# Kernel optimization log

Measured on AMD Instinct MI355X. Metric: run time of the kernel, lower is better.

The kernel has to match this reference:

```python
import jax, jax.numpy as jnp
import numpy as np

D_MODEL, D_K, D_FF, N = 1024, 128, 4096, 8192

def _linear_params(key, fan_in, fan_out):
    # mimic torch nn.Linear default init (uniform +/- 1/sqrt(fan_in))
    k1, k2 = jax.random.split(key)
    bound = 1.0 / np.sqrt(fan_in)
    W = jax.random.uniform(k1, (fan_out, fan_in), jnp.float32, -bound, bound)
    b = jax.random.uniform(k2, (fan_out,), jnp.float32, -bound, bound)
    return W, b

def setup_inputs() -> dict:
    key = jax.random.key(0)
    ks = jax.random.split(key, 7)
    x = jax.random.normal(ks[0], (N, D_MODEL), jnp.float32)
    Wq, bq = _linear_params(ks[1], D_MODEL, D_K)
    Wk, bk = _linear_params(ks[2], D_MODEL, D_K)
    Wv, bv = _linear_params(ks[3], D_MODEL, D_K)
    Wp, bp = _linear_params(ks[4], D_K, D_MODEL)
    W1, b1 = _linear_params(ks[5], D_MODEL, D_FF)
    W2, b2 = _linear_params(ks[6], D_FF, D_MODEL)
    return {"x": x, "Wq": Wq, "bq": bq, "Wk": Wk, "bk": bk, "Wv": Wv, "bv": bv,
            "Wp": Wp, "bp": bp, "W1": W1, "b1": b1, "W2": W2, "b2": b2}

def reference(x, Wq, bq, Wk, bk, Wv, bv, Wp, bp, W1, b1, W2, b2):
    # projections (torch Linear: x @ W.T + b)
    Q = x @ Wq.T + bq            # [n, d_k]
    K = x @ Wk.T + bk            # [n, d_k]
    V = x @ Wv.T + bv            # [n, d_k]
    # linear attention, original evaluation order: (Q @ K^T) @ V
    attn = Q @ K.T               # [n, n]
    context = attn @ V           # [n, d_k]
    out = context @ Wp.T + bp    # [n, d_model]
    x = x + out                  # residual 1
    h = jax.nn.relu(x @ W1.T + b1)  # [n, d_ff]
    return x + (h @ W2.T + b2)   # residual 2
```

## Files before the change

### kernel.cpp

```cpp
#include <hip/hip_runtime.h>


#define MROWS 8192
#define DMODEL 1024
#define DK 128
#define DFF 4096

typedef __attribute__((ext_vector_type(8))) __bf16 bf16x8;
typedef __attribute__((ext_vector_type(4))) float f32x4;

#define BAR()     __builtin_amdgcn_s_barrier()
#define WAITV(n)  asm volatile("s_waitcnt vmcnt(" #n ")" ::: "memory")
#define LGKMC(n)  asm volatile("s_waitcnt lgkmcnt(" #n ")" ::: "memory")
#define SCHED0()  __builtin_amdgcn_sched_barrier(0)
#define GLOAD(src, dst) __builtin_amdgcn_global_load_lds( \
    (const __attribute__((address_space(1))) void*)(src), \
    (__attribute__((address_space(3))) void*)(dst), 16, 0, 0)

#define LDSO(p) ((unsigned)(unsigned long long) \
    (__attribute__((address_space(3))) const char*)(const char*)(p))

__device__ __forceinline__ bf16x8 ldsr(unsigned off) {
    bf16x8 r;
    asm volatile("ds_read_b128 %0, %1" : "=v"(r) : "v"(off));
    return r;
}

__global__ __launch_bounds__(256) void cast_f32_bf16(
    const float* __restrict__ src, __bf16* __restrict__ dst, int n8)
{
    for (int i = blockIdx.x * blockDim.x + threadIdx.x; i < n8;
         i += gridDim.x * blockDim.x) {
        const float4 a = reinterpret_cast<const float4*>(src)[2 * i];
        const float4 b = reinterpret_cast<const float4*>(src)[2 * i + 1];
        bf16x8 o;
        o[0] = (__bf16)a.x; o[1] = (__bf16)a.y; o[2] = (__bf16)a.z; o[3] = (__bf16)a.w;
        o[4] = (__bf16)b.x; o[5] = (__bf16)b.y; o[6] = (__bf16)b.z; o[7] = (__bf16)b.w;
        reinterpret_cast<bf16x8*>(dst)[i] = o;
    }
}

__device__ __forceinline__ void cast_one(const float* s, __bf16* d, int i) {
    const float4 a = reinterpret_cast<const float4*>(s)[2 * i];
    const float4 b = reinterpret_cast<const float4*>(s)[2 * i + 1];
    bf16x8 o;
    o[0] = (__bf16)a.x; o[1] = (__bf16)a.y; o[2] = (__bf16)a.z; o[3] = (__bf16)a.w;
    o[4] = (__bf16)b.x; o[5] = (__bf16)b.y; o[6] = (__bf16)b.z; o[7] = (__bf16)b.w;
    reinterpret_cast<bf16x8*>(d)[i] = o;
}

__global__ __launch_bounds__(256) void cast6(
    const float* __restrict__ s0, __bf16* __restrict__ d0,
    const float* __restrict__ s1, __bf16* __restrict__ d1,
    const float* __restrict__ s2, __bf16* __restrict__ d2,
    const float* __restrict__ s3, __bf16* __restrict__ d3,
    const float* __restrict__ s4, __bf16* __restrict__ d4,
    const float* __restrict__ s5, __bf16* __restrict__ d5)
{
    const int b = blockIdx.x, t = threadIdx.x;
    if      (b <  64)  cast_one(s0, d0, b * 256 + t);
    else if (b < 128)  cast_one(s1, d1, (b - 64) * 256 + t);
    else if (b < 192)  cast_one(s2, d2, (b - 128) * 256 + t);
    else if (b < 256)  cast_one(s3, d3, (b - 192) * 256 + t);
    else if (b < 2304) cast_one(s4, d4, (b - 256) * 256 + t);
    else               cast_one(s5, d5, (b - 2304) * 256 + t);
}

__global__ void pack_bias3(const float* __restrict__ a, const float* __restrict__ b,
                           const float* __restrict__ c, float* __restrict__ o)
{
    const int t = threadIdx.x;
    o[t] = a[t]; o[128 + t] = b[t]; o[256 + t] = c[t];
}

__global__ __launch_bounds__(256) void ffn2_reduce(
    float* __restrict__ y, const __bf16* __restrict__ P0,
    const __bf16* __restrict__ P1, const float* __restrict__ b2, int n8)
{
    for (int i = blockIdx.x * blockDim.x + threadIdx.x; i < n8;
         i += gridDim.x * blockDim.x) {
        const int col0 = (i << 3) & (DMODEL - 1);
        const float4 ba = *reinterpret_cast<const float4*>(&b2[col0]);
        const float4 bb = *reinterpret_cast<const float4*>(&b2[col0 + 4]);
        float4 o0 = reinterpret_cast<const float4*>(y)[2 * i];
        float4 o1 = reinterpret_cast<const float4*>(y)[2 * i + 1];
        const bf16x8 p0 = reinterpret_cast<const bf16x8*>(P0)[i];
        const bf16x8 p1 = reinterpret_cast<const bf16x8*>(P1)[i];
        o0.x += (float)p0[0] + (float)p1[0] + ba.x;
        o0.y += (float)p0[1] + (float)p1[1] + ba.y;
        o0.z += (float)p0[2] + (float)p1[2] + ba.z;
        o0.w += (float)p0[3] + (float)p1[3] + ba.w;
        o1.x += (float)p0[4] + (float)p1[4] + bb.x;
        o1.y += (float)p0[5] + (float)p1[5] + bb.y;
        o1.z += (float)p0[6] + (float)p1[6] + bb.z;
        o1.w += (float)p0[7] + (float)p1[7] + bb.w;
        reinterpret_cast<float4*>(y)[2 * i]     = o0;
        reinterpret_cast<float4*>(y)[2 * i + 1] = o1;
    }
}

template<bool RELU, bool RESID, bool BIAS, bool OUTBF, bool DUAL>
__global__ __launch_bounds__(256) void gemm128(
    const __bf16* __restrict__ A, int lda,
    const __bf16* __restrict__ W,
    const float* __restrict__ bias,
    const float* __restrict__ resid,
    void* __restrict__ Cout, __bf16* __restrict__ Cbf, int ldc, int K)
{
    constexpr int BK = 32;
    __shared__ __bf16 As[128 * BK];
    __shared__ __bf16 Bs[128 * BK];

    const int tid  = threadIdx.x;
    const int lane = tid & 63;
    const int w    = tid >> 6;
    const int wm   = w >> 1;
    const int wn   = w & 1;
    const int fr   = lane & 15;
    const int fq   = lane >> 4;

    const long row0 = (long)blockIdx.y * 128;
    const long col0 = (long)blockIdx.x * 128;

    const int sr = (w << 4) + (lane >> 2);
    const int sc = (lane & 3) << 3;

    const __bf16* gA0 = A + (row0 + sr) * (long)lda + sc;
    const __bf16* gA1 = A + (row0 + 64 + sr) * (long)lda + sc;
    const __bf16* gW0 = W + (col0 + sr) * (long)K + sc;
    const __bf16* gW1 = W + (col0 + 64 + sr) * (long)K + sc;

    __bf16* lA0 = &As[(w << 4) * BK];
    __bf16* lA1 = &As[((w << 4) + 64) * BK];
    __bf16* lB0 = &Bs[(w << 4) * BK];
    __bf16* lB1 = &Bs[((w << 4) + 64) * BK];

    f32x4 acc[4][4] = {};

    for (int k0 = 0; k0 < K; k0 += BK) {
        GLOAD(gA0 + k0, lA0);
        GLOAD(gA1 + k0, lA1);
        GLOAD(gW0 + k0, lB0);
        GLOAD(gW1 + k0, lB1);
        __syncthreads();

        bf16x8 af[4], bfr[4];
        #pragma unroll
        for (int m = 0; m < 4; m++)
            af[m] = *reinterpret_cast<const bf16x8*>(
                &As[(wm * 64 + m * 16 + fr) * BK + fq * 8]);
        #pragma unroll
        for (int n = 0; n < 4; n++)
            bfr[n] = *reinterpret_cast<const bf16x8*>(
                &Bs[(wn * 64 + n * 16 + fr) * BK + fq * 8]);

        #pragma unroll
        for (int m = 0; m < 4; m++)
            #pragma unroll
            for (int n = 0; n < 4; n++)
                acc[m][n] = __builtin_amdgcn_mfma_f32_16x16x32_bf16(
                    af[m], bfr[n], acc[m][n], 0, 0, 0);
        __syncthreads();
    }

    float bc[4];
    #pragma unroll
    for (int n = 0; n < 4; n++)
        bc[n] = BIAS ? bias[col0 + wn * 64 + n * 16 + fr] : 0.0f;
    #pragma unroll
    for (int m = 0; m < 4; m++) {
        #pragma unroll
        for (int j = 0; j < 4; j++) {
            const long r = row0 + wm * 64 + m * 16 + fq * 4 + j;
            #pragma unroll
            for (int n = 0; n < 4; n++) {
                const long c = col0 + wn * 64 + n * 16 + fr;
                float v = acc[m][n][j] + bc[n];
                if constexpr (RESID) v += resid[r * ldc + c];
                if constexpr (RELU)  v = fmaxf(v, 0.0f);
                if constexpr (OUTBF) ((__bf16*)Cout)[r * ldc + c] = (__bf16)v;
                else                 ((float*)Cout)[r * ldc + c] = v;
                if constexpr (DUAL)  Cbf[r * ldc + c] = (__bf16)v;
            }
        }
    }
}

#define RD_B()                                             \
    _Pragma("unroll")                                      \
    for (int n = 0; n < 4; n++) {                          \
        bb[n][0] = ldsr(pB + rb0 + n * 2048);              \
        bb[n][1] = ldsr(pB + rb1 + n * 2048);              \
    }
#define RD_A(m0_, cnt_)                                    \
    _Pragma("unroll")                                      \
    for (int m = m0_; m < m0_ + cnt_; m++) {               \
        a[m][0] = ldsr(pA + rb0 + m * 2048);               \
        a[m][1] = ldsr(pA + rb1 + m * 2048);               \
    }
#define MFMA2(m0_)                                                            \
    _Pragma("unroll")                                                         \
    for (int m = m0_; m < m0_ + 2; m++)                                       \
        _Pragma("unroll")                                                     \
        for (int n = 0; n < 4; n++) {                                         \
            acc[m][n] = __builtin_amdgcn_mfma_f32_16x16x32_bf16(              \
                a[m][0], bb[n][0], acc[m][n], 0, 0, 0);                       \
            acc[m][n] = __builtin_amdgcn_mfma_f32_16x16x32_bf16(              \
                a[m][1], bb[n][1], acc[m][n], 0, 0, 0);                       \
        }

template<bool RELU, bool BIAS>
__global__ __launch_bounds__(256, 2) void gemm256x128(
    const __bf16* __restrict__ A, int lda,
    const __bf16* __restrict__ W, int ldw,
    const float* __restrict__ bias,
    __bf16* __restrict__ Cout, long sstride, int ldc,
    int klen, int nb, int nbx)
{
    __shared__ char lds[49152];

    const int bid = blockIdx.x;
    const int sid = bid / nb;
    const int ib  = bid % nb;
    const int chunk = nb >> 3;
    const int swz   = (ib & 7) * chunk + (ib >> 3);
    const int bx    = swz % nbx;
    const int by    = swz / nbx;

    const long row0 = (long)by * 256;
    const long col0 = (long)bx * 128;

    const __bf16* Ash = A + (long)sid * klen;
    const __bf16* Wsh = W + (long)sid * klen;

    const int tid  = threadIdx.x;
    const int lane = tid & 63;
    const int w    = tid >> 6;
    const int wm   = w >> 1;
    const int wn   = w & 1;
    const int fr   = lane & 15;
    const int fq   = lane >> 4;

    const int scole = ((lane & 7) ^ (lane >> 3)) << 3;
    const __bf16* gA = Ash + (row0 + w * 8 + (lane >> 3)) * (long)lda + scole;
    const __bf16* gB = Wsh + (col0 + w * 8 + (lane >> 3)) * (long)ldw + scole;

    char* ldsc = &lds[0];
    const unsigned lbase = LDSO(ldsc);
    const int nt = klen >> 6;

    auto stage = [&](int t) {
        const __bf16* ap = gA + (long)t * 64;
        const __bf16* bp = gB + (long)t * 64;
        #pragma unroll
        for (int r = 0; r < 8; r++)
            GLOAD(ap + (long)(32 * r) * lda, ldsc + r * 4096 + (w << 10));
        #pragma unroll
        for (int r = 0; r < 4; r++)
            GLOAD(bp + (long)(32 * r) * ldw, ldsc + 32768 + r * 4096 + (w << 10));
    };

    const unsigned rb0 = fr * 128 + ((fq * 16) ^ ((fr & 7) << 4));
    const unsigned rb1 = fr * 128 + ((64 + fq * 16) ^ ((fr & 7) << 4));
    const unsigned pA = lbase + (wm << 14);
    const unsigned pB = lbase + 32768 + (wn << 13);

    f32x4 acc[8][4] = {};
    bf16x8 a[8][2], bb[4][2];

    for (int t = 0; t < nt; ++t) {
        stage(t);
        WAITV(0);
        BAR();

        RD_B();
        RD_A(0, 8);

        LGKMC(12); SCHED0();
        __builtin_amdgcn_s_setprio(1); MFMA2(0); __builtin_amdgcn_s_setprio(0);
        LGKMC(8); SCHED0();
        __builtin_amdgcn_s_setprio(1); MFMA2(2); __builtin_amdgcn_s_setprio(0);
        LGKMC(4); SCHED0();
        __builtin_amdgcn_s_setprio(1); MFMA2(4); __builtin_amdgcn_s_setprio(0);
        LGKMC(0); SCHED0();
        __builtin_amdgcn_s_setprio(1); MFMA2(6); __builtin_amdgcn_s_setprio(0);

        BAR();
    }

    __bf16* Cb = Cout + (long)sid * sstride;
    float bc[4];
    #pragma unroll
    for (int n = 0; n < 4; n++)
        bc[n] = BIAS ? bias[col0 + wn * 64 + n * 16 + fr] : 0.0f;

    __bf16* sw = reinterpret_cast<__bf16*>(ldsc) + (w << 12);
    const long crow0 = row0 + wm * 128;
    const long ccol0 = col0 + wn * 64;
    #pragma unroll
    for (int half = 0; half < 2; half++) {
        #pragma unroll
        for (int m = 0; m < 4; m++)
            #pragma unroll
            for (int j = 0; j < 4; j++) {
                const int row = m * 16 + fq * 4 + j;
                #pragma unroll
                for (int n = 0; n < 4; n++) {
                    float v = acc[half * 4 + m][n][j] + bc[n];
                    if constexpr (RELU) v = fmaxf(v, 0.0f);
                    sw[row * 64 + n * 16 + fr] = (__bf16)v;
                }
            }
        #pragma unroll
        for (int i = 0; i < 8; i++) {
            const bf16x8 vv = *reinterpret_cast<const bf16x8*>(sw + i * 512 + lane * 8);
            const int r  = half * 64 + i * 8 + (lane >> 3);
            const int cg = (lane & 7) << 3;
            *reinterpret_cast<bf16x8*>(&Cb[(crow0 + r) * (long)ldc + ccol0 + cg]) = vv;
        }
        __builtin_amdgcn_s_waitcnt(0);
    }
}

__global__ __launch_bounds__(256) void ktv_partial(
    const __bf16* __restrict__ Kp, const __bf16* __restrict__ Vp,
    int ld, float* __restrict__ part)
{
    __shared__ float ks[32][DK];
    __shared__ float vs[32][DK];
    const int tid = threadIdx.x;
    const int ti  = tid >> 4;
    const int tj  = tid & 15;
    float acc[8][8] = {};
    const long base = (long)blockIdx.x * 128;

    for (int n0 = 0; n0 < 128; n0 += 32) {
        for (int t = tid; t < 512; t += 256) {
            const int r  = t >> 4;
            const int cc = (t & 15) << 3;
            const bf16x8 k8 = *reinterpret_cast<const bf16x8*>(
                &Kp[(base + n0 + r) * (long)ld + cc]);
            const bf16x8 v8 = *reinterpret_cast<const bf16x8*>(
                &Vp[(base + n0 + r) * (long)ld + cc]);
            #pragma unroll
            for (int u = 0; u < 8; u++) {
                ks[r][cc + u] = (float)k8[u];
                vs[r][cc + u] = (float)v8[u];
            }
        }
        __syncthreads();
        for (int n = 0; n < 32; n++) {
            float kk[8], vv[8];
            #pragma unroll
            for (int i = 0; i < 8; i++) kk[i] = ks[n][(ti << 3) + i];
            #pragma unroll
            for (int j = 0; j < 8; j++) vv[j] = vs[n][(tj << 3) + j];
            #pragma unroll
            for (int i = 0; i < 8; i++)
                #pragma unroll
                for (int j = 0; j < 8; j++)
                    acc[i][j] = fmaf(kk[i], vv[j], acc[i][j]);
        }
        __syncthreads();
    }

    float* dst = &part[(long)blockIdx.x * (DK * DK)];
    #pragma unroll
    for (int i = 0; i < 8; i++) {
        const int ig = (ti << 3) + i;
        *reinterpret_cast<float4*>(&dst[ig * DK + (tj << 3)]) =
            make_float4(acc[i][0], acc[i][1], acc[i][2], acc[i][3]);
        *reinterpret_cast<float4*>(&dst[ig * DK + (tj << 3) + 4]) =
            make_float4(acc[i][4], acc[i][5], acc[i][6], acc[i][7]);
    }
}

__global__ __launch_bounds__(256) void ktv_reduce(
    const float* __restrict__ part, __bf16* __restrict__ ktvT)
{
    const int t = blockIdx.x * 256 + threadIdx.x;
    const int i = t >> 7;
    const int j = t & 127;
    float s = 0.0f;
    for (int b = 0; b < 64; b++) s += part[(long)b * (DK * DK) + t];
    ktvT[j * DK + i] = (__bf16)s;
}

extern "C" void kernel_launch(void* const* d_in, const int* in_sizes, int n_in,
                              void* d_out, int out_size, void* d_ws, size_t ws_size,
                              hipStream_t stream) {
    const float* x  = (const float*)d_in[0];
    const float* Wq = (const float*)d_in[1];
    const float* bq = (const float*)d_in[2];
    const float* Wk = (const float*)d_in[3];
    const float* bk = (const float*)d_in[4];
    const float* Wv = (const float*)d_in[5];
    const float* bv = (const float*)d_in[6];
    const float* Wp = (const float*)d_in[7];
    const float* bp = (const float*)d_in[8];
    const float* W1 = (const float*)d_in[9];
    const float* b1 = (const float*)d_in[10];
    const float* W2 = (const float*)d_in[11];
    const float* b2 = (const float*)d_in[12];
    float* out = (float*)d_out;

    char* ws = (char*)d_ws;
    const size_t MB = 1ull << 20;
    __bf16* xb    = (__bf16*)(ws);
    __bf16* P0b   = (__bf16*)(ws);
    __bf16* P1b   = P0b + (long)MROWS * DMODEL;
    __bf16* x2b   = (__bf16*)(ws +  34 * MB);
    __bf16* Hb    = (__bf16*)(ws +  51 * MB);
    __bf16* QKVb  = (__bf16*)(ws + 119 * MB);
    __bf16* W1b   = (__bf16*)(ws + 126 * MB);
    __bf16* W2b   = (__bf16*)(ws + 135 * MB);
    __bf16* Wqkvb = (__bf16*)(ws + 144 * MB);
    __bf16* Wpb   = (__bf16*)(ws + 145 * MB);
    float*  Part  = (float*) (ws + 146 * MB);
    __bf16* KtvTb = (__bf16*)(ws + 151 * MB);
    __bf16* Ctxb  = (__bf16*)(ws + 152 * MB);
    float*  bqkvf = (float*) (ws + 155 * MB);

    const dim3 blk(256);

    cast_f32_bf16<<<2048, blk, 0, stream>>>(x, xb, MROWS * DMODEL / 8);
    cast6<<<4352, blk, 0, stream>>>(
        Wq, Wqkvb, Wk, Wqkvb + DK * DMODEL, Wv, Wqkvb + 2 * DK * DMODEL,
        Wp, Wpb, W1, W1b, W2, W2b);
    pack_bias3<<<1, 128, 0, stream>>>(bq, bk, bv, bqkvf);

    gemm128<false,false,true,true,false><<<dim3(3, 64), blk, 0, stream>>>(
        xb, DMODEL, Wqkvb, bqkvf, nullptr, QKVb, nullptr, 3 * DK, DMODEL);

    ktv_partial<<<64, blk, 0, stream>>>(QKVb + DK, QKVb + 2 * DK, 3 * DK, Part);
    ktv_reduce <<<64, blk, 0, stream>>>(Part, KtvTb);

    gemm128<false,false,false,true,false><<<dim3(1, 64), blk, 0, stream>>>(
        QKVb, 3 * DK, KtvTb, nullptr, nullptr, Ctxb, nullptr, DK, DK);

    gemm128<false,true,true,false,true><<<dim3(8, 64), blk, 0, stream>>>(
        Ctxb, DK, Wpb, bp, x, out, x2b, DMODEL, DK);

    gemm256x128<true,true><<<1024, blk, 0, stream>>>(
        x2b, DMODEL, W1b, DMODEL, b1, Hb, 0, DFF, DMODEL, 1024, DFF / 128);

    gemm256x128<false,false><<<512, blk, 0, stream>>>(
        Hb, DFF, W2b, DFF, nullptr, P0b,
        (long)MROWS * DMODEL, DMODEL, DFF / 2, 256, DMODEL / 128);

    ffn2_reduce<<<2048, blk, 0, stream>>>(out, P0b, P1b, b2, MROWS * DMODEL / 8);
}
```

Measured before the change: 228.2 us.

## Double-buffer FFN GEMM K-loop and fold KtV into output projection weights

The FFN GEMM now uses a K-step of 32 with two LDS buffers, prefetching the next tile while computing the current one, so each iteration needs one barrier instead of two. The XOR swizzle is dropped in favour of a plain 64-byte row layout, which may bring back LDS bank conflicts. Separately, the attention path reassociates Q(KᵀV)Wpᵀ as Q((KᵀV)Wpᵀ): a small 1024x128 matrix is computed once, which removes the 8192-row context GEMM and its intermediate buffer.

```diff
diff --git a/kernel.cpp b/kernel.cpp
--- a/kernel.cpp
+++ b/kernel.cpp
@@ -186,31 +186,16 @@
     }
 }
 
-#define RD_B()                                             \
-    _Pragma("unroll")                                      \
-    for (int n = 0; n < 4; n++) {                          \
-        bb[n][0] = ldsr(pB + rb0 + n * 2048);              \
-        bb[n][1] = ldsr(pB + rb1 + n * 2048);              \
-    }
-#define RD_A(m0_, cnt_)                                    \
-    _Pragma("unroll")                                      \
-    for (int m = m0_; m < m0_ + cnt_; m++) {               \
-        a[m][0] = ldsr(pA + rb0 + m * 2048);               \
-        a[m][1] = ldsr(pA + rb1 + m * 2048);               \
-    }
-#define MFMA2(m0_)                                                            \
+#define MFMA2S(m0_)                                                           \
     _Pragma("unroll")                                                         \
     for (int m = m0_; m < m0_ + 2; m++)                                       \
         _Pragma("unroll")                                                     \
-        for (int n = 0; n < 4; n++) {                                         \
+        for (int n = 0; n < 4; n++)                                           \
             acc[m][n] = __builtin_amdgcn_mfma_f32_16x16x32_bf16(              \
-                a[m][0], bb[n][0], acc[m][n], 0, 0, 0);                       \
-            acc[m][n] = __builtin_amdgcn_mfma_f32_16x16x32_bf16(              \
-                a[m][1], bb[n][1], acc[m][n], 0, 0, 0);                       \
-        }
+                a[m], bb[n], acc[m][n], 0, 0, 0);
 
 template<bool RELU, bool BIAS>
-__global__ __launch_bounds__(256, 2) void gemm256x128(
+__global__ __launch_bounds__(256, 2) void gemm_ffn(
     const __bf16* __restrict__ A, int lda,
     const __bf16* __restrict__ W, int ldw,
     const float* __restrict__ bias,
@@ -241,52 +226,55 @@
     const int fr   = lane & 15;
     const int fq   = lane >> 4;
 
-    const int scole = ((lane & 7) ^ (lane >> 3)) << 3;
-    const __bf16* gA = Ash + (row0 + w * 8 + (lane >> 3)) * (long)lda + scole;
-    const __bf16* gB = Wsh + (col0 + w * 8 + (lane >> 3)) * (long)ldw + scole;
+    const __bf16* gA = Ash + (row0 + w * 16 + (lane >> 2)) * (long)lda
+                       + ((lane & 3) << 3);
+    const __bf16* gB = Wsh + (col0 + w * 16 + (lane >> 2)) * (long)ldw
+                       + ((lane & 3) << 3);
 
     char* ldsc = &lds[0];
     const unsigned lbase = LDSO(ldsc);
-    const int nt = klen >> 6;
-
-    auto stage = [&](int t) {
-        const __bf16* ap = gA + (long)t * 64;
-        const __bf16* bp = gB + (long)t * 64;
-        #pragma unroll
-        for (int r = 0; r < 8; r++)
-            GLOAD(ap + (long)(32 * r) * lda, ldsc + r * 4096 + (w << 10));
+    const int nt = klen >> 5;
+
+    auto stage = [&](int u, unsigned boff) {
+        const __bf16* ap = gA + (long)u * 32;
+        const __bf16* bp = gB + (long)u * 32;
         #pragma unroll
         for (int r = 0; r < 4; r++)
-            GLOAD(bp + (long)(32 * r) * ldw, ldsc + 32768 + r * 4096 + (w << 10));
+            GLOAD(ap + (long)(64 * r) * lda, ldsc + boff + r * 4096 + (w << 10));
+        #pragma unroll
+        for (int r = 0; r < 2; r++)
+            GLOAD(bp + (long)(64 * r) * ldw,
+                  ldsc + boff + 16384 + r * 4096 + (w << 10));
     };
 
-    const unsigned rb0 = fr * 128 + ((fq * 16) ^ ((fr & 7) << 4));
-    const unsigned rb1 = fr * 128 + ((64 + fq * 16) ^ ((fr & 7) << 4));
-    const unsigned pA = lbase + (wm << 14);
-    const unsigned pB = lbase + 32768 + (wn << 13);
-
+    const unsigned rb = fr * 64 + fq * 16;
     f32x4 acc[8][4] = {};
-    bf16x8 a[8][2], bb[4][2];
-
+    bf16x8 a[8], bb[4];
+
+    stage(0, 0);
     for (int t = 0; t < nt; ++t) {
-        stage(t);
+        const unsigned boff = (unsigned)(t & 1) * 24576u;
         WAITV(0);
         BAR();
-
-        RD_B();
-        RD_A(0, 8);
-
-        LGKMC(12); SCHED0();
-        __builtin_amdgcn_s_setprio(1); MFMA2(0); __builtin_amdgcn_s_setprio(0);
-        LGKMC(8); SCHED0();
-        __builtin_amdgcn_s_setprio(1); MFMA2(2); __builtin_amdgcn_s_setprio(0);
+        if (t + 1 < nt) stage(t + 1, 24576u - boff);
+
+        const unsigned pA = lbase + boff + (wm << 13);
+        const unsigned pB = lbase + boff + 16384u + (wn << 12);
+        #pragma unroll
+        for (int n = 0; n < 4; n++) bb[n] = ldsr(pB + rb + n * 1024);
+        #pragma unroll
+        for (int m = 0; m < 8; m++) a[m] = ldsr(pA + rb + m * 1024);
+
+        LGKMC(6); SCHED0();
+        __builtin_amdgcn_s_setprio(1); MFMA2S(0); __builtin_amdgcn_s_setprio(0);
         LGKMC(4); SCHED0();
-        __builtin_amdgcn_s_setprio(1); MFMA2(4); __builtin_amdgcn_s_setprio(0);
+        __builtin_amdgcn_s_setprio(1); MFMA2S(2); __builtin_amdgcn_s_setprio(0);
+        LGKMC(2); SCHED0();
+        __builtin_amdgcn_s_setprio(1); MFMA2S(4); __builtin_amdgcn_s_setprio(0);
         LGKMC(0); SCHED0();
-        __builtin_amdgcn_s_setprio(1); MFMA2(6); __builtin_amdgcn_s_setprio(0);
-
-        BAR();
-    }
+        __builtin_amdgcn_s_setprio(1); MFMA2S(6); __builtin_amdgcn_s_setprio(0);
+    }
+    BAR();
 
     __bf16* Cb = Cout + (long)sid * sstride;
     float bc[4];
@@ -318,7 +306,7 @@
             const int cg = (lane & 7) << 3;
             *reinterpret_cast<bf16x8*>(&Cb[(crow0 + r) * (long)ldc + ccol0 + cg]) = vv;
         }
-        __builtin_amdgcn_s_waitcnt(0);
+        LGKMC(0);
     }
 }
 
@@ -376,14 +364,12 @@
 }
 
 __global__ __launch_bounds__(256) void ktv_reduce(
-    const float* __restrict__ part, __bf16* __restrict__ ktvT)
+    const float* __restrict__ part, __bf16* __restrict__ ktvR)
 {
     const int t = blockIdx.x * 256 + threadIdx.x;
-    const int i = t >> 7;
-    const int j = t & 127;
     float s = 0.0f;
     for (int b = 0; b < 64; b++) s += part[(long)b * (DK * DK) + t];
-    ktvT[j * DK + i] = (__bf16)s;
+    ktvR[t] = (__bf16)s;
 }
 
 extern "C" void kernel_launch(void* const* d_in, const int* in_sizes, int n_in,
@@ -417,8 +403,8 @@
     __bf16* Wqkvb = (__bf16*)(ws + 144 * MB);
     __bf16* Wpb   = (__bf16*)(ws + 145 * MB);
     float*  Part  = (float*) (ws + 146 * MB);
-    __bf16* KtvTb = (__bf16*)(ws + 151 * MB);
-    __bf16* Ctxb  = (__bf16*)(ws + 152 * MB);
+    __bf16* KtvRb = (__bf16*)(ws + 151 * MB);
+    __bf16* MtB   = (__bf16*)(ws + 152 * MB);
     float*  bqkvf = (float*) (ws + 155 * MB);
 
     const dim3 blk(256);
@@ -433,18 +419,18 @@
         xb, DMODEL, Wqkvb, bqkvf, nullptr, QKVb, nullptr, 3 * DK, DMODEL);
 
     ktv_partial<<<64, blk, 0, stream>>>(QKVb + DK, QKVb + 2 * DK, 3 * DK, Part);
-    ktv_reduce <<<64, blk, 0, stream>>>(Part, KtvTb);
-
-    gemm128<false,false,false,true,false><<<dim3(1, 64), blk, 0, stream>>>(
-        QKVb, 3 * DK, KtvTb, nullptr, nullptr, Ctxb, nullptr, DK, DK);
+    ktv_reduce <<<64, blk, 0, stream>>>(Part, KtvRb);
+
+    gemm128<false,false,false,true,false><<<dim3(1, 8), blk, 0, stream>>>(
+        Wpb, DK, KtvRb, nullptr, nullptr, MtB, nullptr, DK, DK);
 
     gemm128<false,true,true,false,true><<<dim3(8, 64), blk, 0, stream>>>(
-        Ctxb, DK, Wpb, bp, x, out, x2b, DMODEL, DK);
-
-    gemm256x128<true,true><<<1024, blk, 0, stream>>>(
+        QKVb, 3 * DK, MtB, bp, x, out, x2b, DMODEL, DK);
+
+    gemm_ffn<true,true><<<1024, blk, 0, stream>>>(
         x2b, DMODEL, W1b, DMODEL, b1, Hb, 0, DFF, DMODEL, 1024, DFF / 128);
 
-    gemm256x128<false,false><<<512, blk, 0, stream>>>(
+    gemm_ffn<false,false><<<512, blk, 0, stream>>>(
         Hb, DFF, W2b, DFF, nullptr, P0b,
         (long)MROWS * DMODEL, DMODEL, DFF / 2, 256, DMODEL / 128);
 
```

New measurement: 244.9 us. +7.3%, slower.
